# Performance work log

Hardware: AMD Instinct MI355X
Metric: run time of the kernel (lower is better)

The kernel has to match this reference:

```python
import jax, jax.numpy as jnp
import numpy as np

B, K, D = 16, 2048, 512
INNER = 2 * D  # expand * d_model
KW = 5        # d_conv=4 bumped to odd 5
EPS = 1e-5


def setup_inputs() -> dict:
    key = jax.random.key(0)
    ks = jax.random.split(key, 8)
    x = jax.random.normal(ks[0], (B, K, D), dtype=jnp.float32)
    norm_w = jnp.ones((D,), dtype=jnp.float32)
    Wa = jax.random.normal(ks[1], (INNER, D), dtype=jnp.float32) * (1.0 / np.sqrt(D))
    Wb = jax.random.normal(ks[2], (INNER, D), dtype=jnp.float32) * (1.0 / np.sqrt(D))
    conv_w = jax.random.normal(ks[3], (INNER, 1, KW), dtype=jnp.float32) * (1.0 / np.sqrt(KW))
    conv_b = jax.random.normal(ks[4], (INNER,), dtype=jnp.float32) * 0.01
    alpha = jnp.zeros((INNER,), dtype=jnp.float32)
    beta = jnp.ones((INNER,), dtype=jnp.float32)
    gamma = jnp.ones((INNER,), dtype=jnp.float32)
    delta = jnp.zeros((INNER,), dtype=jnp.float32)
    Wout = jax.random.normal(ks[5], (D, INNER), dtype=jnp.float32) * (1.0 / np.sqrt(INNER))
    return {"x": x, "norm_w": norm_w, "Wa": Wa, "Wb": Wb, "conv_w": conv_w,
            "conv_b": conv_b, "alpha": alpha, "beta": beta, "gamma": gamma,
            "delta": delta, "Wout": Wout}


def _rmsnorm(x, w):
    var = jnp.mean(x * x, axis=-1, keepdims=True)
    return x * jax.lax.rsqrt(var + EPS) * w


def _dwconv(a, conv_w, conv_b):
    # a: [B, INNER, K]; depthwise conv, 'same' padding (pad = KW//2)
    y = jax.lax.conv_general_dilated(
        a, conv_w,
        window_strides=(1,), padding=[(KW // 2, KW // 2)],
        dimension_numbers=("NCH", "OIH", "NCH"),
        feature_group_count=INNER)
    return y + conv_b[None, :, None]


def _selective_scan(u, alpha, beta, gamma, delta):
    # u: [B, K, INNER]; per-channel LTI recurrence s_t = a*s_{t-1} + b*u_t, y_t = g*s_t + d*u_t
    a = jax.nn.sigmoid(alpha)

    def step(s, ut):
        s = a * s + beta * ut
        return s, gamma * s + delta * ut

    u_t = jnp.transpose(u, (1, 0, 2))  # [K, B, INNER]
    s0 = jnp.zeros((u.shape[0], u.shape[2]), dtype=u.dtype)
    _, ys = jax.lax.scan(step, s0, u_t)
    return jnp.transpose(ys, (1, 0, 2))  # [B, K, INNER]


def reference(x, norm_w, Wa, Wb, conv_w, conv_b, alpha, beta, gamma, delta, Wout):
    h = _rmsnorm(x, norm_w)
    a = jnp.einsum("bkd,id->bki", h, Wa)  # [B,K,INNER]
    b = jnp.einsum("bkd,id->bki", h, Wb)
    a = jnp.transpose(a, (0, 2, 1))       # [B,INNER,K]
    a = _dwconv(a, conv_w, conv_b)
    a = jnp.transpose(a, (0, 2, 1))       # [B,K,INNER]
    a = jax.nn.silu(a)
    s = _selective_scan(a, alpha, beta, gamma, delta)
    g = s * b
    y = jnp.einsum("bki,di->bkd", g, Wout)
    return x + y
```

## Files before the change

### kernel.cpp

```cpp
#include <hip/hip_runtime.h>
#include <stdint.h>

#define B_ 16
#define K_ 2048
#define D_ 512
#define INNER_ 1024
#define M_ (B_*K_)
#define KW_ 5
#define EPS_ 1e-5f
#define NC_ 64
#define CL_ (K_/NC_)

typedef __attribute__((ext_vector_type(8))) short short8;
typedef __attribute__((ext_vector_type(4))) float f32x4;
typedef __attribute__((ext_vector_type(8))) float f32x8;

typedef const __attribute__((address_space(1))) unsigned int* gas_u32;
typedef __attribute__((address_space(3))) unsigned int* las_u32;

static __device__ __forceinline__ float bf2f(unsigned short u) {
    unsigned int v = ((unsigned int)u) << 16;
    return __builtin_bit_cast(float, v);
}
static __device__ __forceinline__ unsigned short f2bf(float f) {
    unsigned int x = __builtin_bit_cast(unsigned int, f);
    unsigned int r = (x + 0x7FFFu + ((x >> 16) & 1u)) >> 16;
    return (unsigned short)r;
}
static __device__ __forceinline__ f32x8 cvt8(short8 v) {
    f32x8 f;
    #pragma unroll
    for (int j = 0; j < 8; ++j) f[j] = bf2f((unsigned short)v[j]);
    return f;
}

__global__ __launch_bounds__(256) void k_wconv(const float* __restrict__ Wa,
                                               const float* __restrict__ Wb,
                                               const float* __restrict__ Wout,
                                               unsigned short* __restrict__ Wcat,
                                               unsigned short* __restrict__ WoutB) {
    const int NW = INNER_ * D_;
    int idx = blockIdx.x * 256 + threadIdx.x;
    if (idx < NW)            Wcat[idx]       = f2bf(Wa[idx]);
    else if (idx < 2 * NW)   Wcat[idx]       = f2bf(Wb[idx - NW]);
    else                     WoutB[idx-2*NW] = f2bf(Wout[idx - 2*NW]);
}

__global__ __launch_bounds__(256) void k_rmsnorm(const float* __restrict__ x,
                                                 const float* __restrict__ w,
                                                 unsigned short* __restrict__ h) {
    int row  = blockIdx.x * 4 + (threadIdx.x >> 6);
    int lane = threadIdx.x & 63;
    const float4* xr = (const float4*)(x + (size_t)row * D_);
    float4 v0 = xr[lane];
    float4 v1 = xr[64 + lane];
    float ss = v0.x*v0.x + v0.y*v0.y + v0.z*v0.z + v0.w*v0.w
             + v1.x*v1.x + v1.y*v1.y + v1.z*v1.z + v1.w*v1.w;
    #pragma unroll
    for (int off = 32; off; off >>= 1) ss += __shfl_xor(ss, off, 64);
    float r = rsqrtf(ss * (1.0f / D_) + EPS_);
    const float4* wv = (const float4*)w;
    float4 w0 = wv[lane], w1 = wv[64 + lane];
    ushort4 o0, o1;
    o0.x = f2bf(v0.x * r * w0.x); o0.y = f2bf(v0.y * r * w0.y);
    o0.z = f2bf(v0.z * r * w0.z); o0.w = f2bf(v0.w * r * w0.w);
    o1.x = f2bf(v1.x * r * w1.x); o1.y = f2bf(v1.y * r * w1.y);
    o1.z = f2bf(v1.z * r * w1.z); o1.w = f2bf(v1.w * r * w1.w);
    ushort4* hr = (ushort4*)(h + (size_t)row * D_);
    hr[lane]      = o0;
    hr[64 + lane] = o1;
}

template<int EPI>
__global__ __launch_bounds__(512) void k_gemm256(
    const unsigned short* __restrict__ A,
    const unsigned short* __restrict__ Bw,
    void* __restrict__ Cv,
    const float* __restrict__ Xadd,
    int Kd, int Nld)
{
    __shared__ __align__(16) unsigned short lA[2][256 * 64];
    __shared__ __align__(16) unsigned short lB[2][256 * 64];
    const int tid  = threadIdx.x;
    const int w    = tid >> 6, lane = tid & 63;
    const int wr   = w >> 2,   wc   = w & 3;

    const int nwg = gridDim.x * gridDim.y;
    const int fid = blockIdx.y * gridDim.x + blockIdx.x;
    const int swz = (fid & 7) * (nwg >> 3) + (fid >> 3);
    const int m0  = (swz / gridDim.y) * 256;
    const int n0  = (swz % gridDim.y) * 256;

    const int srow = w * 8 + (lane >> 3);
    const int scol = ((lane & 7) ^ (lane >> 3)) << 3;
    const int NT   = Kd >> 6;

    auto stage = [&](int t, int buf) {
        const int kt = t << 6;
        const unsigned short* ga = A  + (size_t)(m0 + srow) * Kd + kt + scol;
        const unsigned short* gb = Bw + (size_t)(n0 + srow) * Kd + kt + scol;
        #pragma unroll
        for (int j = 0; j < 4; ++j) {
            __builtin_amdgcn_global_load_lds((gas_u32)(ga + (size_t)j * 64 * Kd),
                                             (las_u32)(&lA[buf][(j * 64 + w * 8) * 64]), 16, 0, 0);
            __builtin_amdgcn_global_load_lds((gas_u32)(gb + (size_t)j * 64 * Kd),
                                             (las_u32)(&lB[buf][(j * 64 + w * 8) * 64]), 16, 0, 0);
        }
    };

    f32x4 acc[8][4];
    #pragma unroll
    for (int m = 0; m < 8; ++m)
        #pragma unroll
        for (int n = 0; n < 4; ++n) acc[m][n] = (f32x4){0.f, 0.f, 0.f, 0.f};

    const int lrow = lane & 15;
    const int hb   = (lane >> 4) << 4;
    const int xr   = (lrow & 7) << 4;

    stage(0, 0);
    stage(1, 1);

    for (int t = 0; t < NT; ++t) {
        const int buf = t & 1;
        if (t + 1 < NT) asm volatile("s_waitcnt vmcnt(8)" ::: "memory");
        else            asm volatile("s_waitcnt vmcnt(0)" ::: "memory");
        __builtin_amdgcn_s_barrier();

        const char* pa = (const char*)lA[buf];
        const char* pb = (const char*)lB[buf];

        short8 a0[8], b0[4];
        #pragma unroll
        for (int m = 0; m < 8; ++m)
            a0[m] = *(const short8*)(pa + (wr*128 + m*16 + lrow) * 128 + (hb ^ xr));
        #pragma unroll
        for (int n = 0; n < 4; ++n)
            b0[n] = *(const short8*)(pb + (wc*64 + n*16 + lrow) * 128 + (hb ^ xr));

        __builtin_amdgcn_s_setprio(1);
        #pragma unroll
        for (int m = 0; m < 8; ++m)
            #pragma unroll
            for (int n = 0; n < 4; ++n)
                acc[m][n] = __builtin_amdgcn_mfma_f32_16x16x32_bf16(a0[m], b0[n], acc[m][n], 0, 0, 0);
        __builtin_amdgcn_s_setprio(0);

        short8 a1[8], b1[4];
        #pragma unroll
        for (int m = 0; m < 8; ++m)
            a1[m] = *(const short8*)(pa + (wr*128 + m*16 + lrow) * 128 + ((64 + hb) ^ xr));
        #pragma unroll
        for (int n = 0; n < 4; ++n)
            b1[n] = *(const short8*)(pb + (wc*64 + n*16 + lrow) * 128 + ((64 + hb) ^ xr));

        asm volatile("s_waitcnt lgkmcnt(0)" ::: "memory");
        __builtin_amdgcn_s_barrier();
        if (t + 2 < NT) stage(t + 2, buf);

        __builtin_amdgcn_s_setprio(1);
        #pragma unroll
        for (int m = 0; m < 8; ++m)
            #pragma unroll
            for (int n = 0; n < 4; ++n)
                acc[m][n] = __builtin_amdgcn_mfma_f32_16x16x32_bf16(a1[m], b1[n], acc[m][n], 0, 0, 0);
        __builtin_amdgcn_s_setprio(0);
    }

    #pragma unroll
    for (int m = 0; m < 8; ++m) {
        int mrow = m0 + wr*128 + m*16 + ((lane >> 4) << 2);
        #pragma unroll
        for (int n = 0; n < 4; ++n) {
            int ncol = n0 + wc*64 + n*16 + (lane & 15);
            f32x4 v = acc[m][n];
            #pragma unroll
            for (int r = 0; r < 4; ++r) {
                size_t off = (size_t)(mrow + r) * Nld + ncol;
                if (EPI == 0) ((unsigned short*)Cv)[off] = f2bf(v[r]);
                else          ((float*)Cv)[off] = Xadd[off] + v[r];
            }
        }
    }
}

__global__ __launch_bounds__(256) void k_prefix(const float* __restrict__ alpha,
                                                const float* __restrict__ sEnd,
                                                float* __restrict__ sPre) {
    int idx = blockIdx.x * 256 + threadIdx.x;
    int b = idx >> 10, i = idx & 1023;
    float Aa = 1.f / (1.f + __expf(-alpha[i]));
    float Ap = Aa;
    #pragma unroll
    for (int t = 0; t < 5; ++t) Ap = Ap * Ap;
    float s = 0.f;
    for (int c = 0; c < NC_; ++c) {
        size_t off = ((size_t)(b * NC_ + c)) * INNER_ + i;
        sPre[off] = s;
        s = s * Ap + sEnd[off];
    }
}

template<int PASS>
__global__ __launch_bounds__(256) void k_scan(
    const unsigned short* __restrict__ ab,
    const float* __restrict__ conv_w, const float* __restrict__ conv_b,
    const float* __restrict__ alpha,  const float* __restrict__ beta,
    const float* __restrict__ gamma,  const float* __restrict__ delta,
    float* __restrict__ sEnd, const float* __restrict__ sPre,
    unsigned short* __restrict__ g)
{
    const int tid = threadIdx.x;
    const int c   = blockIdx.x * 2 + (tid >> 7);
    const int b   = blockIdx.y;
    const int ch  = (tid & 127) * 8;

    f32x8 w0, w1, w2, w3, w4, bias, Aa, bet, gam, del;
    #pragma unroll
    for (int j = 0; j < 8; ++j) {
        int i = ch + j;
        w0[j] = conv_w[i*KW_+0]; w1[j] = conv_w[i*KW_+1]; w2[j] = conv_w[i*KW_+2];
        w3[j] = conv_w[i*KW_+3]; w4[j] = conv_w[i*KW_+4];
        bias[j] = conv_b[i];
        Aa[j]  = 1.f / (1.f + __expf(-alpha[i]));
        bet[j] = beta[i];
        if (PASS == 1) { gam[j] = gamma[i]; del[j] = delta[i]; }
    }

    const int k0 = c * CL_;
    const size_t rowbase = (size_t)b * K_;

    #define LDV(k) (((unsigned)(k) < (unsigned)K_) \
        ? cvt8(*(const short8*)(ab + (rowbase + (k)) * 2048 + ch)) \
        : (f32x8){0.f,0.f,0.f,0.f,0.f,0.f,0.f,0.f})

    f32x8 am2 = LDV(k0 - 2), am1 = LDV(k0 - 1), a0v = LDV(k0), ap1 = LDV(k0 + 1);

    f32x8 s;
    if (PASS == 1) {
        s = *(const f32x8*)(sPre + ((size_t)(b * NC_ + c)) * INNER_ + ch);
    } else {
        #pragma unroll
        for (int j = 0; j < 8; ++j) s[j] = 0.f;
    }

    #pragma unroll 2
    for (int kk = 0; kk < CL_; ++kk) {
        int k = k0 + kk;
        f32x8 ap2 = LDV(k + 2);
        f32x8 v = w0*am2 + w1*am1 + w2*a0v + w3*ap1 + w4*ap2 + bias;
        f32x8 u;
        #pragma unroll
        for (int j = 0; j < 8; ++j) u[j] = v[j] / (1.f + __expf(-v[j]));
        s = Aa * s + bet * u;
        if (PASS == 1) {
            f32x8 bv = cvt8(*(const short8*)(ab + (rowbase + k) * 2048 + INNER_ + ch));
            f32x8 gv = (gam * s + del * u) * bv;
            short8 o;
            #pragma unroll
            for (int j = 0; j < 8; ++j) o[j] = (short)f2bf(gv[j]);
            *(short8*)(g + (rowbase + k) * INNER_ + ch) = o;
        }
        am2 = am1; am1 = a0v; a0v = ap1; ap1 = ap2;
    }
    if (PASS == 0)
        *(f32x8*)(sEnd + ((size_t)(b * NC_ + c)) * INNER_ + ch) = s;
    #undef LDV
}

extern "C" void kernel_launch(void* const* d_in, const int* in_sizes, int n_in,
                              void* d_out, int out_size, void* d_ws, size_t ws_size,
                              hipStream_t stream) {
    const float* x      = (const float*)d_in[0];
    const float* norm_w = (const float*)d_in[1];
    const float* Wa     = (const float*)d_in[2];
    const float* Wb     = (const float*)d_in[3];
    const float* conv_w = (const float*)d_in[4];
    const float* conv_b = (const float*)d_in[5];
    const float* alpha  = (const float*)d_in[6];
    const float* beta   = (const float*)d_in[7];
    const float* gamma  = (const float*)d_in[8];
    const float* delta  = (const float*)d_in[9];
    const float* Wout   = (const float*)d_in[10];
    float* out = (float*)d_out;

    char* ws = (char*)d_ws;
    unsigned short* h    = (unsigned short*)ws; ws += (size_t)M_ * D_ * 2;
    unsigned short* Wcat = (unsigned short*)ws; ws += (size_t)2048 * 512 * 2;
    unsigned short* WoB  = (unsigned short*)ws; ws += (size_t)512 * 1024 * 2;
    unsigned short* abb  = (unsigned short*)ws; ws += (size_t)M_ * 2048 * 2;
    unsigned short* g    = (unsigned short*)ws; ws += (size_t)M_ * 1024 * 2;
    float* sEnd          = (float*)ws;          ws += (size_t)B_ * NC_ * INNER_ * 4;
    float* sPre          = (float*)ws;          ws += (size_t)B_ * NC_ * INNER_ * 4;

    k_wconv  <<<6144, 256, 0, stream>>>(Wa, Wb, Wout, Wcat, WoB);
    k_rmsnorm<<<M_ / 4, 256, 0, stream>>>(x, norm_w, h);
    k_gemm256<0><<<dim3(M_ / 256, 2048 / 256), 512, 0, stream>>>(h, Wcat, abb, nullptr, 512, 2048);
    k_scan<0><<<dim3(NC_ / 2, B_), 256, 0, stream>>>(abb, conv_w, conv_b, alpha, beta, gamma, delta, sEnd, nullptr, g);
    k_prefix<<<64, 256, 0, stream>>>(alpha, sEnd, sPre);
    k_scan<1><<<dim3(NC_ / 2, B_), 256, 0, stream>>>(abb, conv_w, conv_b, alpha, beta, gamma, delta, sEnd, sPre, g);
    k_gemm256<1><<<dim3(M_ / 256, 512 / 256), 512, 0, stream>>>(g, WoB, out, x, 1024, 512);
}
```

Before: 358.5 us.

## Interleave GEMM global-to-LDS staging with MFMA in four sub-phases per k-tile

Rewrites the bf16 GEMM main loop so the next k-tile's loads are issued in four pieces, one between each of four MFMA sub-blocks, instead of one bulk stage two tiles ahead. Register fragments are cut to 4 A rows at a time, which lowers VGPR pressure. The goal is to spread memory traffic evenly over compute and raise occupancy. In exchange it adds many more barriers per iteration and shortens prefetch distance to one tile. The vmcnt wait counts must stay matched to the staging order, which makes it fragile.

```diff
diff --git a/kernel.cpp b/kernel.cpp
--- a/kernel.cpp
+++ b/kernel.cpp
@@ -95,16 +95,24 @@
     const int scol = ((lane & 7) ^ (lane >> 3)) << 3;
     const int NT   = Kd >> 6;
 
-    auto stage = [&](int t, int buf) {
+    auto stagePair = [&](int t, int buf, int which) {
         const int kt = t << 6;
-        const unsigned short* ga = A  + (size_t)(m0 + srow) * Kd + kt + scol;
-        const unsigned short* gb = Bw + (size_t)(n0 + srow) * Kd + kt + scol;
-        #pragma unroll
-        for (int j = 0; j < 4; ++j) {
-            __builtin_amdgcn_global_load_lds((gas_u32)(ga + (size_t)j * 64 * Kd),
-                                             (las_u32)(&lA[buf][(j * 64 + w * 8) * 64]), 16, 0, 0);
-            __builtin_amdgcn_global_load_lds((gas_u32)(gb + (size_t)j * 64 * Kd),
-                                             (las_u32)(&lB[buf][(j * 64 + w * 8) * 64]), 16, 0, 0);
+        if (which < 2) {
+            const unsigned short* gb = Bw + (size_t)(n0 + srow) * Kd + kt + scol;
+            #pragma unroll
+            for (int jj = 0; jj < 2; ++jj) {
+                int j = which * 2 + jj;
+                __builtin_amdgcn_global_load_lds((gas_u32)(gb + (size_t)j * 64 * Kd),
+                    (las_u32)(&lB[buf][(j * 64 + w * 8) * 64]), 16, 0, 0);
+            }
+        } else {
+            const unsigned short* ga = A + (size_t)(m0 + srow) * Kd + kt + scol;
+            #pragma unroll
+            for (int jj = 0; jj < 2; ++jj) {
+                int j = (which - 2) + jj * 2;
+                __builtin_amdgcn_global_load_lds((gas_u32)(ga + (size_t)j * 64 * Kd),
+                    (las_u32)(&lA[buf][(j * 64 + w * 8) * 64]), 16, 0, 0);
+            }
         }
     };
 
@@ -118,53 +126,81 @@
     const int hb   = (lane >> 4) << 4;
     const int xr   = (lrow & 7) << 4;
 
-    stage(0, 0);
-    stage(1, 1);
+    stagePair(0, 0, 0); stagePair(0, 0, 1); stagePair(0, 0, 2); stagePair(0, 0, 3);
+    asm volatile("s_waitcnt vmcnt(2)" ::: "memory");
+    __builtin_amdgcn_s_barrier();
 
     for (int t = 0; t < NT; ++t) {
-        const int buf = t & 1;
-        if (t + 1 < NT) asm volatile("s_waitcnt vmcnt(8)" ::: "memory");
-        else            asm volatile("s_waitcnt vmcnt(0)" ::: "memory");
-        __builtin_amdgcn_s_barrier();
-
-        const char* pa = (const char*)lA[buf];
-        const char* pb = (const char*)lB[buf];
-
-        short8 a0[8], b0[4];
-        #pragma unroll
-        for (int m = 0; m < 8; ++m)
-            a0[m] = *(const short8*)(pa + (wr*128 + m*16 + lrow) * 128 + (hb ^ xr));
+        const int cur = t & 1, nxt = cur ^ 1;
+        const bool more = (t + 1 < NT);
+        const char* pa = (const char*)lA[cur];
+        const char* pb = (const char*)lB[cur];
+        short8 a[4], b[4];
+
+        #pragma unroll
+        for (int m = 0; m < 4; ++m)
+            a[m] = *(const short8*)(pa + (wr*128 + m*16 + lrow) * 128 + (hb ^ xr));
         #pragma unroll
         for (int n = 0; n < 4; ++n)
-            b0[n] = *(const short8*)(pb + (wc*64 + n*16 + lrow) * 128 + (hb ^ xr));
-
+            b[n] = *(const short8*)(pb + (wc*64 + n*16 + lrow) * 128 + (hb ^ xr));
+        if (more) stagePair(t + 1, nxt, 0);
+        __builtin_amdgcn_s_barrier();
         __builtin_amdgcn_s_setprio(1);
         #pragma unroll
-        for (int m = 0; m < 8; ++m)
+        for (int m = 0; m < 4; ++m)
             #pragma unroll
             for (int n = 0; n < 4; ++n)
-                acc[m][n] = __builtin_amdgcn_mfma_f32_16x16x32_bf16(a0[m], b0[n], acc[m][n], 0, 0, 0);
+                acc[m][n] = __builtin_amdgcn_mfma_f32_16x16x32_bf16(a[m], b[n], acc[m][n], 0, 0, 0);
         __builtin_amdgcn_s_setprio(0);
-
-        short8 a1[8], b1[4];
-        #pragma unroll
-        for (int m = 0; m < 8; ++m)
-            a1[m] = *(const short8*)(pa + (wr*128 + m*16 + lrow) * 128 + ((64 + hb) ^ xr));
+        if (more) asm volatile("s_waitcnt vmcnt(2)" ::: "memory");
+        else      asm volatile("s_waitcnt vmcnt(0)" ::: "memory");
+        __builtin_amdgcn_s_barrier();
+
+        #pragma unroll
+        for (int m = 0; m < 4; ++m)
+            a[m] = *(const short8*)(pa + (wr*128 + 64 + m*16 + lrow) * 128 + (hb ^ xr));
+        if (more) stagePair(t + 1, nxt, 1);
+        __builtin_amdgcn_s_barrier();
+        __builtin_amdgcn_s_setprio(1);
+        #pragma unroll
+        for (int m = 0; m < 4; ++m)
+            #pragma unroll
+            for (int n = 0; n < 4; ++n)
+                acc[4+m][n] = __builtin_amdgcn_mfma_f32_16x16x32_bf16(a[m], b[n], acc[4+m][n], 0, 0, 0);
+        __builtin_amdgcn_s_setprio(0);
+        __builtin_amdgcn_s_barrier();
+
+        #pragma unroll
+        for (int m = 0; m < 4; ++m)
+            a[m] = *(const short8*)(pa + (wr*128 + m*16 + lrow) * 128 + ((64 + hb) ^ xr));
         #pragma unroll
         for (int n = 0; n < 4; ++n)
-            b1[n] = *(const short8*)(pb + (wc*64 + n*16 + lrow) * 128 + ((64 + hb) ^ xr));
-
-        asm volatile("s_waitcnt lgkmcnt(0)" ::: "memory");
-        __builtin_amdgcn_s_barrier();
-        if (t + 2 < NT) stage(t + 2, buf);
-
+            b[n] = *(const short8*)(pb + (wc*64 + n*16 + lrow) * 128 + ((64 + hb) ^ xr));
+        if (more) stagePair(t + 1, nxt, 2);
+        __builtin_amdgcn_s_barrier();
         __builtin_amdgcn_s_setprio(1);
         #pragma unroll
-        for (int m = 0; m < 8; ++m)
+        for (int m = 0; m < 4; ++m)
             #pragma unroll
             for (int n = 0; n < 4; ++n)
-                acc[m][n] = __builtin_amdgcn_mfma_f32_16x16x32_bf16(a1[m], b1[n], acc[m][n], 0, 0, 0);
+                acc[m][n] = __builtin_amdgcn_mfma_f32_16x16x32_bf16(a[m], b[n], acc[m][n], 0, 0, 0);
         __builtin_amdgcn_s_setprio(0);
+        __builtin_amdgcn_s_barrier();
+
+        #pragma unroll
+        for (int m = 0; m < 4; ++m)
+            a[m] = *(const short8*)(pa + (wr*128 + 64 + m*16 + lrow) * 128 + ((64 + hb) ^ xr));
+        if (more) stagePair(t + 1, nxt, 3);
+        __builtin_amdgcn_s_barrier();
+        __builtin_amdgcn_s_setprio(1);
+        #pragma unroll
+        for (int m = 0; m < 4; ++m)
+            #pragma unroll
+            for (int n = 0; n < 4; ++n)
+                acc[4+m][n] = __builtin_amdgcn_mfma_f32_16x16x32_bf16(a[m], b[n], acc[4+m][n], 0, 0, 0);
+        __builtin_amdgcn_s_setprio(0);
+        if (more) asm volatile("s_waitcnt vmcnt(2)" ::: "memory");
+        __builtin_amdgcn_s_barrier();
     }
 
     #pragma unroll
```

After: 359.0 us. About the same (+0.2%).
